# Kernel optimization log

Measured on AMD Instinct MI355X. Metric: run time of the kernel, lower is better.

Reference implementation:

```python
import jax, jax.numpy as jnp
import numpy as np

B, T, C = 1, 4096, 1024
NH, NKV, HD = 16, 4, 64
N_REP = NH // NKV
WIN = 1024
EPS = 1e-5
ROPE_THETA = 10000.0


def setup_inputs() -> dict:
    key = jax.random.key(0)
    ks = jax.random.split(key, 6)
    s = 1.0 / np.sqrt(C)
    x = jax.random.normal(ks[0], (B, T, C), jnp.float32)
    wq = jax.random.normal(ks[1], (NH * HD, C), jnp.float32) * s
    wk = jax.random.normal(ks[2], (NKV * HD, C), jnp.float32) * s
    wv = jax.random.normal(ks[3], (NKV * HD, C), jnp.float32) * s
    wo = jax.random.normal(ks[4], (C, NH * HD), jnp.float32) * (1.0 / np.sqrt(NH * HD))
    q_norm_w = jnp.ones((HD,), jnp.float32)
    k_norm_w = jnp.ones((HD,), jnp.float32)
    # RoPE tables: (T, HD//2)
    inv_freq = 1.0 / (ROPE_THETA ** (np.arange(0, HD, 2, dtype=np.float32) / HD))
    ang = np.outer(np.arange(T, dtype=np.float32), inv_freq)
    freqs_cos = jnp.asarray(np.cos(ang), jnp.float32)
    freqs_sin = jnp.asarray(np.sin(ang), jnp.float32)
    return {"x": x, "wq": wq, "wk": wk, "wv": wv, "wo": wo,
            "q_norm_w": q_norm_w, "k_norm_w": k_norm_w,
            "freqs_cos": freqs_cos, "freqs_sin": freqs_sin}


def _rmsnorm(v, w):
    # RMSNorm over last dim (per-head)
    return v * jax.lax.rsqrt(jnp.mean(v * v, axis=-1, keepdims=True) + EPS) * w


def _rope(v, cos, sin):
    # v: (B, T, H, HD); interleaved complex rotation, matching torch polar freqs_cis
    vr, vi = v[..., 0::2], v[..., 1::2]
    c = cos[None, :, None, :]
    s = sin[None, :, None, :]
    out_r = vr * c - vi * s
    out_i = vr * s + vi * c
    return jnp.stack([out_r, out_i], axis=-1).reshape(v.shape)


def reference(x, wq, wk, wv, wo, q_norm_w, k_norm_w, freqs_cos, freqs_sin):
    xq = jnp.einsum('btc,dc->btd', x, wq).reshape(B, T, NH, HD)
    xk = jnp.einsum('btc,dc->btd', x, wk).reshape(B, T, NKV, HD)
    xv = jnp.einsum('btc,dc->btd', x, wv).reshape(B, T, NKV, HD)
    # per-head QK RMSNorm
    xq = _rmsnorm(xq, q_norm_w)
    xk = _rmsnorm(xk, k_norm_w)
    # RoPE
    xq = _rope(xq, freqs_cos, freqs_sin)
    xk = _rope(xk, freqs_cos, freqs_sin)
    # GQA: expand kv heads
    xk = jnp.repeat(xk, N_REP, axis=2)  # (B, T, NH, HD)
    xv = jnp.repeat(xv, N_REP, axis=2)
    scale = 1.0 / np.sqrt(HD)
    scores = jnp.einsum('bthd,bshd->bhts', xq, xk) * scale
    i = jnp.arange(T)[:, None]
    j = jnp.arange(T)[None, :]
    mask = (i >= j) & (i - j < WIN)  # causal + sliding window
    scores = jnp.where(mask[None, None], scores, -jnp.inf)
    attn = jax.nn.softmax(scores, axis=-1)
    y = jnp.einsum('bhts,bshd->bthd', attn, xv).reshape(B, T, NH * HD)
    return jnp.einsum('btd,cd->btc', y, wo)
```

## Files before the change

kernel.cpp:

```cpp
#include <hip/hip_runtime.h>
#include <hip/hip_bf16.h>


#define WIN_SZ 1024

typedef __attribute__((ext_vector_type(8))) short short8;
typedef __attribute__((ext_vector_type(8))) unsigned short ushort8;
typedef __attribute__((ext_vector_type(4))) float f32x4;
typedef __attribute__((ext_vector_type(16))) float f32x16;

#define GLOAD_LDS16(g, s)                                              \
  __builtin_amdgcn_global_load_lds(                                    \
      (const __attribute__((address_space(1))) unsigned int*)(g),      \
      (__attribute__((address_space(3))) unsigned int*)(s), 16, 0, 0)

__device__ __forceinline__ unsigned short f2bf(float f) {
  union { float f; unsigned u; } v; v.f = f;
  unsigned r = v.u + 0x7fffu + ((v.u >> 16) & 1u);
  return (unsigned short)(r >> 16);
}

__device__ __forceinline__ float bf2f(unsigned short b) {
  union { unsigned u; float f; } v; v.u = ((unsigned)b) << 16; return v.f;
}

__device__ __forceinline__ unsigned pk2bf(float lo, float hi) {
  __hip_bfloat162 h = __float22bfloat162_rn(make_float2(lo, hi));
  union { __hip_bfloat162 h; unsigned u; } c; c.h = h; return c.u;
}

__device__ __forceinline__ short8 frag4(unsigned w0, unsigned w1, unsigned w2, unsigned w3) {
  union { unsigned u[4]; short8 s; } x;
  x.u[0] = w0; x.u[1] = w1; x.u[2] = w2; x.u[3] = w3; return x.s;
}

__global__ __launch_bounds__(256) void k_f2b_all(const float* __restrict__ x,
                                                 const float* __restrict__ wq,
                                                 const float* __restrict__ wk,
                                                 const float* __restrict__ wv,
                                                 const float* __restrict__ wo,
                                                 unsigned short* __restrict__ xb,
                                                 unsigned short* __restrict__ wqkvb,
                                                 unsigned short* __restrict__ wob) {
  int q = blockIdx.x * 256 + threadIdx.x;
  const float* src;
  unsigned short* dst;
  int off;
  if (q < 1048576) { src = x; dst = xb; off = q; }
  else if (q < 1310720) { src = wq; dst = wqkvb; off = q - 1048576; }
  else if (q < 1376256) { src = wk; dst = wqkvb + 1024 * 1024; off = q - 1310720; }
  else if (q < 1441792) { src = wv; dst = wqkvb + 1280 * 1024; off = q - 1376256; }
  else { src = wo; dst = wob; off = q - 1441792; }
  float4 v = ((const float4*)src)[off];
  ushort4 o;
  o.x = f2bf(v.x); o.y = f2bf(v.y); o.z = f2bf(v.z); o.w = f2bf(v.w);
  ((ushort4*)dst)[off] = o;
}

template <int BF16OUT>
__global__ __launch_bounds__(256) void k_gemmN64(const unsigned short* __restrict__ A,
                                                 const unsigned short* __restrict__ B,
                                                 void* __restrict__ Cv,
                                                 int M, int N, int K, int nblk) {
  __shared__ unsigned short As[2][128 * 64];
  __shared__ unsigned short Bs[2][64 * 64];
  const int id = blockIdx.x;
  const int chunk = gridDim.x >> 3;
  const int swz = (id & 7) * chunk + (id >> 3);
  const int n_idx = swz % nblk, m_idx = swz / nblk;
  const int m0 = m_idx * 128, n0 = n_idx * 64;

  const int tid = threadIdx.x;
  const int w = tid >> 6, l = tid & 63;
  const int wr = w >> 1, wc = w & 1;
  const int r = l & 15, g = l >> 4;
  const int lr = l >> 3, lc = l & 7;
  const int srowb = w * 32, browb = w * 16;

  f32x4 acc[4][2];
#pragma unroll
  for (int i = 0; i < 4; i++)
#pragma unroll
    for (int j = 0; j < 2; j++) acc[i][j] = {0.f, 0.f, 0.f, 0.f};

  const unsigned short* Ag = A + (size_t)(m0 + srowb + lr) * K + lc * 8;
  const unsigned short* Bg = B + (size_t)(n0 + browb + lr) * K + lc * 8;

  auto stage = [&](int buf, int k0) {
#pragma unroll
    for (int it = 0; it < 4; it++)
      GLOAD_LDS16(Ag + (size_t)(it * 8) * K + k0, &As[buf][(srowb + it * 8) * 64]);
#pragma unroll
    for (int it = 0; it < 2; it++)
      GLOAD_LDS16(Bg + (size_t)(it * 8) * K + k0, &Bs[buf][(browb + it * 8) * 64]);
  };

  stage(0, 0);
  __syncthreads();
  int cur = 0;
  const int NT = K >> 6;
  for (int t = 0; t < NT; ++t) {
    if (t + 1 < NT) stage(cur ^ 1, (t + 1) << 6);
    const char* Ab = (const char*)As[cur];
    const char* Bb = (const char*)Bs[cur];
#pragma unroll
    for (int kk = 0; kk < 2; kk++) {
      short8 af[4], bfr[2];
#pragma unroll
      for (int mi = 0; mi < 4; mi++)
        af[mi] = *(const short8*)(Ab + (wr * 64 + mi * 16 + r) * 128 + kk * 64 + g * 16);
#pragma unroll
      for (int nj = 0; nj < 2; nj++)
        bfr[nj] = *(const short8*)(Bb + (wc * 32 + nj * 16 + r) * 128 + kk * 64 + g * 16);
#pragma unroll
      for (int mi = 0; mi < 4; mi++)
#pragma unroll
        for (int nj = 0; nj < 2; nj++)
          acc[mi][nj] = __builtin_amdgcn_mfma_f32_16x16x32_bf16(af[mi], bfr[nj], acc[mi][nj], 0, 0, 0);
    }
    __syncthreads();
    cur ^= 1;
  }

#pragma unroll
  for (int mi = 0; mi < 4; mi++)
#pragma unroll
    for (int nj = 0; nj < 2; nj++) {
      int row = m0 + wr * 64 + mi * 16 + g * 4;
      int col = n0 + wc * 32 + nj * 16 + r;
      if (BF16OUT) {
        unsigned short* C = (unsigned short*)Cv;
#pragma unroll
        for (int e = 0; e < 4; e++)
          C[(size_t)(row + e) * N + col] = f2bf(acc[mi][nj][e]);
      } else {
        float* C = (float*)Cv;
#pragma unroll
        for (int e = 0; e < 4; e++)
          C[(size_t)(row + e) * N + col] = acc[mi][nj][e];
      }
    }
}

__global__ __launch_bounds__(256) void k_normrope(const unsigned short* __restrict__ QKV,
                                                  const float* __restrict__ qw,
                                                  const float* __restrict__ kw,
                                                  const float* __restrict__ fc,
                                                  const float* __restrict__ fs,
                                                  unsigned short* __restrict__ Qb,
                                                  unsigned short* __restrict__ Kb,
                                                  unsigned short* __restrict__ Vtg,
                                                  int* __restrict__ ctr) {
  if (blockIdx.x == 0 && threadIdx.x == 0) *ctr = 0;
  int gid = blockIdx.x * 4 + (threadIdx.x >> 6);
  int l = threadIdx.x & 63;
  int t = gid / 24;
  int u = gid - t * 24;
  if (u < 16) {
    float v = bf2f(QKV[(size_t)t * 1536 + u * 64 + l]);
    float ss = v * v;
#pragma unroll
    for (int off = 32; off; off >>= 1) ss += __shfl_xor(ss, off);
    float rms = rsqrtf(ss * (1.0f / 64.0f) + 1e-5f);
    float vn = v * rms * qw[l];
    float c = fc[t * 32 + (l >> 1)], s = fs[t * 32 + (l >> 1)];
    float p = __shfl_xor(vn, 1);
    float out = (l & 1) ? (p * s + vn * c) : (vn * c - p * s);
    Qb[(size_t)t * 1024 + u * 64 + l] = f2bf(out * 0.1803368801111204f);
  } else if (u < 20) {
    int hh = u - 16;
    float v = bf2f(QKV[(size_t)t * 1536 + 1024 + hh * 64 + l]);
    float ss = v * v;
#pragma unroll
    for (int off = 32; off; off >>= 1) ss += __shfl_xor(ss, off);
    float rms = rsqrtf(ss * (1.0f / 64.0f) + 1e-5f);
    float vn = v * rms * kw[l];
    float c = fc[t * 32 + (l >> 1)], s = fs[t * 32 + (l >> 1)];
    float p = __shfl_xor(vn, 1);
    float out = (l & 1) ? (p * s + vn * c) : (vn * c - p * s);
    Kb[(size_t)t * 256 + hh * 64 + l] = f2bf(out);
  } else {
    int hh = u - 20;
    Vtg[(size_t)(hh * 64 + l) * 4096 + t] = QKV[(size_t)t * 1536 + 1280 + hh * 64 + l];
  }
}

__global__ __launch_bounds__(512, 4) void k_attn5(const unsigned short* __restrict__ Qb,
                                                  const unsigned short* __restrict__ Kb,
                                                  const unsigned short* __restrict__ Vtg,
                                                  unsigned short* __restrict__ Yb,
                                                  int* __restrict__ ctr) {
  __shared__ char smem[4 * 8192 + 1024];
  __shared__ int s_unit;
  char* stage = smem;
  float* Obuf = (float*)smem;
  float* ml = (float*)(smem + 32768);

  const int tid = threadIdx.x, w = tid >> 6, l = tid & 63;
  const int hh = w & 3, half = w >> 2;
  const int l31 = l & 31, hi = l >> 5, l15 = l & 15;

  const int sb = tid >> 7;
  const int su = tid & 127;
  const int srow = su >> 1;
  const int sg = (su & 1) * 4;
  const int sbase = sb * 8192 + (srow & 31) * 256;
  const int srx = (srow & 15) << 4;
  const int srh = (srow >> 5) * 128;
  const bool isV = sb & 1;
  const int kbase = half * 16384;
  const int vbase = kbase + 8192;

  for (;;) {
    __syncthreads();
    if (tid == 0) s_unit = atomicAdd(ctr, 1);
    __syncthreads();
    const int u = s_unit;
    if (u >= 512) break;
    const int qi = 127 - (u >> 2);
    const int hk = u & 3;
    const int q0 = qi * 32;
    const int h = hk * 4 + hh;
    const int qrow = q0 + l31;

    int jlo = q0 - (WIN_SZ - 1);
    if (jlo < 0) jlo = 0;
    jlo &= ~63;
    const int jlast = ((q0 + 31) >> 6) << 6;
    const int nt = ((jlast - jlo) >> 6) + 1;
    const int nh0 = (nt + 1) >> 1;

    const unsigned short* gK = Kb + (size_t)srow * 256 + hk * 64 + sg * 8;
    const unsigned short* gV = Vtg + (size_t)(hk * 64 + srow) * 4096 + sg * 8;

    short8 qf[4];
#pragma unroll
    for (int ks = 0; ks < 4; ks++)
      qf[ks] = *(const short8*)(Qb + (size_t)qrow * 1024 + h * 64 + ks * 16 + hi * 8);

    f32x16 accO0, accO1;
#pragma unroll
    for (int i = 0; i < 16; i++) { accO0[i] = 0.f; accO1[i] = 0.f; }
    float m = -1e30f, lsum = 0.f;

    ushort8 pre[4];
    auto prefetch = [&](int s) {
      int jt0 = jlo + (s << 6);
      int t1 = nh0 + s;
      int jt1 = (t1 < nt) ? (jlo + (t1 << 6)) : jlo;
      int jt = (sb >= 2) ? jt1 : jt0;
      if (!isV) {
        const unsigned short* g = gK + (size_t)jt * 256;
#pragma unroll
        for (int e = 0; e < 4; e++) pre[e] = *(const ushort8*)(g + e * 8);
      } else {
        const unsigned short* g = gV + jt;
#pragma unroll
        for (int e = 0; e < 4; e++) pre[e] = *(const ushort8*)(g + e * 8);
      }
    };
    prefetch(0);

    for (int s = 0; s < nh0; ++s) {
      __syncthreads();
#pragma unroll
      for (int e = 0; e < 4; e++) {
        int dst = sbase + ((srh + (sg + e) * 16) ^ srx);
        *(ushort8*)(stage + dst) = pre[e];
      }
      __syncthreads();
      if (s + 1 < nh0) prefetch(s + 1);

      const int myt = half ? (nh0 + s) : s;
      if (myt < nt) {
        const int jt = jlo + (myt << 6);

        f32x16 st0, st1;
#pragma unroll
        for (int i = 0; i < 16; i++) { st0[i] = 0.f; st1[i] = 0.f; }
        __builtin_amdgcn_s_setprio(1);
#pragma unroll
        for (int ks = 0; ks < 4; ks++) {
          int colb = ks * 32 + hi * 16;
          short8 kf0 = *(const short8*)(stage + kbase + l31 * 256 + (colb ^ (l15 << 4)));
          st0 = __builtin_amdgcn_mfma_f32_32x32x16_bf16(kf0, qf[ks], st0, 0, 0, 0);
          short8 kf1 = *(const short8*)(stage + kbase + l31 * 256 + ((128 + colb) ^ (l15 << 4)));
          st1 = __builtin_amdgcn_mfma_f32_32x32x16_bf16(kf1, qf[ks], st1, 0, 0, 0);
        }
        __builtin_amdgcn_s_setprio(0);

        if (jt + 63 > q0 || (q0 + 31) - jt >= WIN_SZ) {
          const int jb = jt + hi * 4;
#pragma unroll
          for (int rg = 0; rg < 16; rg++) {
            int j0 = jb + (rg & 3) + 8 * (rg >> 2);
            if (!((j0 <= qrow) && (qrow - j0 < WIN_SZ))) st0[rg] = -3.0e38f;
            int j1 = j0 + 32;
            if (!((j1 <= qrow) && (qrow - j1 < WIN_SZ))) st1[rg] = -3.0e38f;
          }
        }

        float mx = st0[0];
#pragma unroll
        for (int rg = 1; rg < 16; rg++) mx = fmaxf(mx, st0[rg]);
#pragma unroll
        for (int rg = 0; rg < 16; rg++) mx = fmaxf(mx, st1[rg]);
        mx = fmaxf(mx, __shfl_xor(mx, 32));
        if (!__all(mx <= m + 8.0f)) {
          float mnew = fmaxf(m, mx);
          float alpha = exp2f(m - mnew);
#pragma unroll
          for (int rg = 0; rg < 16; rg++) { accO0[rg] *= alpha; accO1[rg] *= alpha; }
          lsum *= alpha;
          m = mnew;
        }
        float ps = 0.f;
#pragma unroll
        for (int rg = 0; rg < 16; rg++) { st0[rg] = exp2f(st0[rg] - m); ps += st0[rg]; }
#pragma unroll
        for (int rg = 0; rg < 16; rg++) { st1[rg] = exp2f(st1[rg] - m); ps += st1[rg]; }
        lsum += ps;

        unsigned pd0[2][4], pd1[2][4];
#pragma unroll
        for (int b = 0; b < 4; b++) {
          pd0[0][b] = pk2bf(st0[4 * b], st0[4 * b + 1]);
          pd1[0][b] = pk2bf(st0[4 * b + 2], st0[4 * b + 3]);
          pd0[1][b] = pk2bf(st1[4 * b], st1[4 * b + 1]);
          pd1[1][b] = pk2bf(st1[4 * b + 2], st1[4 * b + 3]);
        }

        __builtin_amdgcn_s_setprio(1);
#pragma unroll
        for (int jj = 0; jj < 2; jj++) {
#pragma unroll
          for (int ks2 = 0; ks2 < 2; ks2++) {
            unsigned a0 = pd0[jj][2 * ks2], a1 = pd0[jj][2 * ks2 + 1];
            unsigned b0 = pd1[jj][2 * ks2], b1 = pd1[jj][2 * ks2 + 1];
            unsigned a0x = __shfl_xor(a0, 32), a1x = __shfl_xor(a1, 32);
            unsigned b0x = __shfl_xor(b0, 32), b1x = __shfl_xor(b1, 32);
            unsigned w0 = hi ? a1x : a0;
            unsigned w1 = hi ? b1x : b0;
            unsigned w2 = hi ? a1 : a0x;
            unsigned w3 = hi ? b1 : b0x;
            short8 pf = frag4(w0, w1, w2, w3);
            int colb2 = jj * 64 + ks2 * 32 + hi * 16;
            short8 vf0 = *(const short8*)(stage + vbase + l31 * 256 + (colb2 ^ (l15 << 4)));
            accO0 = __builtin_amdgcn_mfma_f32_32x32x16_bf16(vf0, pf, accO0, 0, 0, 0);
            short8 vf1 = *(const short8*)(stage + vbase + l31 * 256 + ((128 + colb2) ^ (l15 << 4)));
            accO1 = __builtin_amdgcn_mfma_f32_32x32x16_bf16(vf1, pf, accO1, 0, 0, 0);
          }
        }
        __builtin_amdgcn_s_setprio(0);
      }
    }

    lsum += __shfl_xor(lsum, 32);
    __syncthreads();
    if (half == 1) {
#pragma unroll
      for (int dd = 0; dd < 2; dd++) {
        const f32x16& a = dd ? accO1 : accO0;
#pragma unroll
        for (int rg = 0; rg < 16; rg++) {
          int d = dd * 32 + 8 * (rg >> 2) + 4 * hi + (rg & 3);
          Obuf[(hh * 64 + d) * 32 + l31] = a[rg];
        }
      }
      if (!hi) { ml[(hh * 2 + 0) * 32 + l31] = m; ml[(hh * 2 + 1) * 32 + l31] = lsum; }
    }
    __syncthreads();
    if (half == 0) {
      float m1 = ml[(hh * 2 + 0) * 32 + l31];
      float l1 = ml[(hh * 2 + 1) * 32 + l31];
      float ms = fmaxf(m, m1);
      float a0 = exp2f(m - ms), a1 = exp2f(m1 - ms);
      float inv = 1.0f / (lsum * a0 + l1 * a1);
      a0 *= inv; a1 *= inv;
#pragma unroll
      for (int dd = 0; dd < 2; dd++) {
        const f32x16& a = dd ? accO1 : accO0;
#pragma unroll
        for (int b = 0; b < 4; b++) {
          float o[4];
#pragma unroll
          for (int e = 0; e < 4; e++) {
            int d = dd * 32 + 8 * b + 4 * hi + e;
            o[e] = a[4 * b + e] * a0 + Obuf[(hh * 64 + d) * 32 + l31] * a1;
          }
          union { unsigned uu[2]; ushort4 v; } ov;
          ov.uu[0] = pk2bf(o[0], o[1]);
          ov.uu[1] = pk2bf(o[2], o[3]);
          *(ushort4*)(Yb + (size_t)qrow * 1024 + h * 64 + dd * 32 + b * 8 + hi * 4) = ov.v;
        }
      }
    }
  }
}

extern "C" void kernel_launch(void* const* d_in, const int* in_sizes, int n_in,
                              void* d_out, int out_size, void* d_ws, size_t ws_size,
                              hipStream_t stream) {
  const float* x = (const float*)d_in[0];
  const float* wq = (const float*)d_in[1];
  const float* wk = (const float*)d_in[2];
  const float* wv = (const float*)d_in[3];
  const float* wo = (const float*)d_in[4];
  const float* qw = (const float*)d_in[5];
  const float* kw = (const float*)d_in[6];
  const float* fc = (const float*)d_in[7];
  const float* fs = (const float*)d_in[8];
  float* out = (float*)d_out;

  char* p = (char*)d_ws;
  auto alloc = [&](size_t b) {
    char* q = p;
    p += (b + 255) & ~(size_t)255;
    return q;
  };
  unsigned short* xb = (unsigned short*)alloc((size_t)4096 * 1024 * 2);
  unsigned short* wqkvb = (unsigned short*)alloc((size_t)1536 * 1024 * 2);
  unsigned short* wob = (unsigned short*)alloc((size_t)1024 * 1024 * 2);
  unsigned short* QKVb = (unsigned short*)alloc((size_t)4096 * 1536 * 2);
  unsigned short* Qb = (unsigned short*)alloc((size_t)4096 * 1024 * 2);
  unsigned short* Kb = (unsigned short*)alloc((size_t)4096 * 256 * 2);
  unsigned short* Vtg = (unsigned short*)alloc((size_t)256 * 4096 * 2);
  unsigned short* Yb = (unsigned short*)alloc((size_t)4096 * 1024 * 2);
  int* ctr = (int*)alloc(256);

  k_f2b_all<<<6656, 256, 0, stream>>>(x, wq, wk, wv, wo, xb, wqkvb, wob);
  k_gemmN64<1><<<768, 256, 0, stream>>>(xb, wqkvb, QKVb, 4096, 1536, 1024, 24);
  k_normrope<<<24576, 256, 0, stream>>>(QKVb, qw, kw, fc, fs, Qb, Kb, Vtg, ctr);
  k_attn5<<<384, 512, 0, stream>>>(Qb, Kb, Vtg, Yb, ctr);
  k_gemmN64<0><<<512, 256, 0, stream>>>(Yb, wob, out, 4096, 1024, 1024, 16);
}
```

Measured before the change: 135.0 us.

## Replace persistent atomic scheduler with static pairing and double-buffered LDS staging

The attention kernel drops its persistent atomic work queue and launches one block per (query tile, kv head) unit. Each block id maps to a unit so that long and short causal tiles are paired. K/V staging now uses two LDS buffers of 32KB each, so the next tile is stored while the current one is computed, which removes one barrier per iteration. The cost is twice the LDS footprint per block, which may limit how many blocks fit on a CU, and the static mapping may balance work less evenly than the dynamic queue.

```diff
diff --git a/kernel.cpp b/kernel.cpp
--- a/kernel.cpp
+++ b/kernel.cpp
@@ -149,9 +149,7 @@
                                                   const float* __restrict__ fs,
                                                   unsigned short* __restrict__ Qb,
                                                   unsigned short* __restrict__ Kb,
-                                                  unsigned short* __restrict__ Vtg,
-                                                  int* __restrict__ ctr) {
-  if (blockIdx.x == 0 && threadIdx.x == 0) *ctr = 0;
+                                                  unsigned short* __restrict__ Vtg) {
   int gid = blockIdx.x * 4 + (threadIdx.x >> 6);
   int l = threadIdx.x & 63;
   int t = gid / 24;
@@ -185,20 +183,34 @@
   }
 }
 
-__global__ __launch_bounds__(512, 4) void k_attn5(const unsigned short* __restrict__ Qb,
+__global__ __launch_bounds__(512, 4) void k_attn6(const unsigned short* __restrict__ Qb,
                                                   const unsigned short* __restrict__ Kb,
                                                   const unsigned short* __restrict__ Vtg,
-                                                  unsigned short* __restrict__ Yb,
-                                                  int* __restrict__ ctr) {
-  __shared__ char smem[4 * 8192 + 1024];
-  __shared__ int s_unit;
+                                                  unsigned short* __restrict__ Yb) {
+  __shared__ char smem[65536 + 1024];
   char* stage = smem;
   float* Obuf = (float*)smem;
-  float* ml = (float*)(smem + 32768);
+  float* ml = (float*)(smem + 65536);
+
+  const int id = blockIdx.x;
+  const int cupair = id & 255, sel = id >> 8;
+  int qi = cupair >> 1;
+  if (sel) qi = 127 - qi;
+  const int hk = (cupair & 1) * 2 + sel;
+  const int q0 = qi * 32;
 
   const int tid = threadIdx.x, w = tid >> 6, l = tid & 63;
   const int hh = w & 3, half = w >> 2;
+  const int h = hk * 4 + hh;
   const int l31 = l & 31, hi = l >> 5, l15 = l & 15;
+  const int qrow = q0 + l31;
+
+  int jlo = q0 - (WIN_SZ - 1);
+  if (jlo < 0) jlo = 0;
+  jlo &= ~63;
+  const int jlast = ((q0 + 31) >> 6) << 6;
+  const int nt = ((jlast - jlo) >> 6) + 1;
+  const int nh0 = (nt + 1) >> 1;
 
   const int sb = tid >> 7;
   const int su = tid & 127;
@@ -208,191 +220,177 @@
   const int srx = (srow & 15) << 4;
   const int srh = (srow >> 5) * 128;
   const bool isV = sb & 1;
-  const int kbase = half * 16384;
-  const int vbase = kbase + 8192;
-
-  for (;;) {
+  const unsigned short* gK = Kb + (size_t)srow * 256 + hk * 64 + sg * 8;
+  const unsigned short* gV = Vtg + (size_t)(hk * 64 + srow) * 4096 + sg * 8;
+
+  short8 qf[4];
+#pragma unroll
+  for (int ks = 0; ks < 4; ks++)
+    qf[ks] = *(const short8*)(Qb + (size_t)qrow * 1024 + h * 64 + ks * 16 + hi * 8);
+
+  f32x16 accO0, accO1;
+#pragma unroll
+  for (int i = 0; i < 16; i++) { accO0[i] = 0.f; accO1[i] = 0.f; }
+  float m = -1e30f, lsum = 0.f;
+
+  ushort8 pre[4];
+  auto prefetch = [&](int s) {
+    int jt0 = jlo + (s << 6);
+    int t1 = nh0 + s;
+    int jt1 = (t1 < nt) ? (jlo + (t1 << 6)) : jlo;
+    int jt = (sb >= 2) ? jt1 : jt0;
+    if (!isV) {
+      const unsigned short* g = gK + (size_t)jt * 256;
+#pragma unroll
+      for (int e = 0; e < 4; e++) pre[e] = *(const ushort8*)(g + e * 8);
+    } else {
+      const unsigned short* g = gV + jt;
+#pragma unroll
+      for (int e = 0; e < 4; e++) pre[e] = *(const ushort8*)(g + e * 8);
+    }
+  };
+  auto store_set = [&](int set) {
+    char* dstb = stage + set * 32768 + sbase;
+#pragma unroll
+    for (int e = 0; e < 4; e++)
+      *(ushort8*)(dstb + ((srh + (sg + e) * 16) ^ srx)) = pre[e];
+  };
+
+  prefetch(0);
+  store_set(0);
+  if (nh0 > 1) prefetch(1);
+  __syncthreads();
+
+  for (int s = 0; s < nh0; ++s) {
+    if (s + 1 < nh0) {
+      store_set((s + 1) & 1);
+      if (s + 2 < nh0) prefetch(s + 2);
+    }
+    const int setoff = (s & 1) * 32768;
+    const int kbase = setoff + half * 16384;
+    const int vbase = kbase + 8192;
+
+    const int myt = half ? (nh0 + s) : s;
+    if (myt < nt) {
+      const int jt = jlo + (myt << 6);
+
+      f32x16 st0, st1;
+#pragma unroll
+      for (int i = 0; i < 16; i++) { st0[i] = 0.f; st1[i] = 0.f; }
+      __builtin_amdgcn_s_setprio(1);
+#pragma unroll
+      for (int ks = 0; ks < 4; ks++) {
+        int colb = ks * 32 + hi * 16;
+        short8 kf0 = *(const short8*)(stage + kbase + l31 * 256 + (colb ^ (l15 << 4)));
+        st0 = __builtin_amdgcn_mfma_f32_32x32x16_bf16(kf0, qf[ks], st0, 0, 0, 0);
+        short8 kf1 = *(const short8*)(stage + kbase + l31 * 256 + ((128 + colb) ^ (l15 << 4)));
+        st1 = __builtin_amdgcn_mfma_f32_32x32x16_bf16(kf1, qf[ks], st1, 0, 0, 0);
+      }
+      __builtin_amdgcn_s_setprio(0);
+
+      if (jt + 63 > q0 || (q0 + 31) - jt >= WIN_SZ) {
+        const int jb = jt + hi * 4;
+#pragma unroll
+        for (int rg = 0; rg < 16; rg++) {
+          int j0 = jb + (rg & 3) + 8 * (rg >> 2);
+          if (!((j0 <= qrow) && (qrow - j0 < WIN_SZ))) st0[rg] = -3.0e38f;
+          int j1 = j0 + 32;
+          if (!((j1 <= qrow) && (qrow - j1 < WIN_SZ))) st1[rg] = -3.0e38f;
+        }
+      }
+
+      float mx = st0[0];
+#pragma unroll
+      for (int rg = 1; rg < 16; rg++) mx = fmaxf(mx, st0[rg]);
+#pragma unroll
+      for (int rg = 0; rg < 16; rg++) mx = fmaxf(mx, st1[rg]);
+      mx = fmaxf(mx, __shfl_xor(mx, 32));
+      if (!__all(mx <= m + 8.0f)) {
+        float mnew = fmaxf(m, mx);
+        float alpha = exp2f(m - mnew);
+#pragma unroll
+        for (int rg = 0; rg < 16; rg++) { accO0[rg] *= alpha; accO1[rg] *= alpha; }
+        lsum *= alpha;
+        m = mnew;
+      }
+      float ps = 0.f;
+#pragma unroll
+      for (int rg = 0; rg < 16; rg++) { st0[rg] = exp2f(st0[rg] - m); ps += st0[rg]; }
+#pragma unroll
+      for (int rg = 0; rg < 16; rg++) { st1[rg] = exp2f(st1[rg] - m); ps += st1[rg]; }
+      lsum += ps;
+
+      unsigned pd0[2][4], pd1[2][4];
+#pragma unroll
+      for (int b = 0; b < 4; b++) {
+        pd0[0][b] = pk2bf(st0[4 * b], st0[4 * b + 1]);
+        pd1[0][b] = pk2bf(st0[4 * b + 2], st0[4 * b + 3]);
+        pd0[1][b] = pk2bf(st1[4 * b], st1[4 * b + 1]);
+        pd1[1][b] = pk2bf(st1[4 * b + 2], st1[4 * b + 3]);
+      }
+
+      __builtin_amdgcn_s_setprio(1);
+#pragma unroll
+      for (int jj = 0; jj < 2; jj++) {
+#pragma unroll
+        for (int ks2 = 0; ks2 < 2; ks2++) {
+          unsigned a0 = pd0[jj][2 * ks2], a1 = pd0[jj][2 * ks2 + 1];
+          unsigned b0 = pd1[jj][2 * ks2], b1 = pd1[jj][2 * ks2 + 1];
+          unsigned a0x = __shfl_xor(a0, 32), a1x = __shfl_xor(a1, 32);
+          unsigned b0x = __shfl_xor(b0, 32), b1x = __shfl_xor(b1, 32);
+          unsigned w0 = hi ? a1x : a0;
+          unsigned w1 = hi ? b1x : b0;
+          unsigned w2 = hi ? a1 : a0x;
+          unsigned w3 = hi ? b1 : b0x;
+          short8 pf = frag4(w0, w1, w2, w3);
+          int colb2 = jj * 64 + ks2 * 32 + hi * 16;
+          short8 vf0 = *(const short8*)(stage + vbase + l31 * 256 + (colb2 ^ (l15 << 4)));
+          accO0 = __builtin_amdgcn_mfma_f32_32x32x16_bf16(vf0, pf, accO0, 0, 0, 0);
+          short8 vf1 = *(const short8*)(stage + vbase + l31 * 256 + ((128 + colb2) ^ (l15 << 4)));
+          accO1 = __builtin_amdgcn_mfma_f32_32x32x16_bf16(vf1, pf, accO1, 0, 0, 0);
+        }
+      }
+      __builtin_amdgcn_s_setprio(0);
+    }
     __syncthreads();
-    if (tid == 0) s_unit = atomicAdd(ctr, 1);
-    __syncthreads();
-    const int u = s_unit;
-    if (u >= 512) break;
-    const int qi = 127 - (u >> 2);
-    const int hk = u & 3;
-    const int q0 = qi * 32;
-    const int h = hk * 4 + hh;
-    const int qrow = q0 + l31;
-
-    int jlo = q0 - (WIN_SZ - 1);
-    if (jlo < 0) jlo = 0;
-    jlo &= ~63;
-    const int jlast = ((q0 + 31) >> 6) << 6;
-    const int nt = ((jlast - jlo) >> 6) + 1;
-    const int nh0 = (nt + 1) >> 1;
-
-    const unsigned short* gK = Kb + (size_t)srow * 256 + hk * 64 + sg * 8;
-    const unsigned short* gV = Vtg + (size_t)(hk * 64 + srow) * 4096 + sg * 8;
-
-    short8 qf[4];
-#pragma unroll
-    for (int ks = 0; ks < 4; ks++)
-      qf[ks] = *(const short8*)(Qb + (size_t)qrow * 1024 + h * 64 + ks * 16 + hi * 8);
-
-    f32x16 accO0, accO1;
-#pragma unroll
-    for (int i = 0; i < 16; i++) { accO0[i] = 0.f; accO1[i] = 0.f; }
-    float m = -1e30f, lsum = 0.f;
-
-    ushort8 pre[4];
-    auto prefetch = [&](int s) {
-      int jt0 = jlo + (s << 6);
-      int t1 = nh0 + s;
-      int jt1 = (t1 < nt) ? (jlo + (t1 << 6)) : jlo;
-      int jt = (sb >= 2) ? jt1 : jt0;
-      if (!isV) {
-        const unsigned short* g = gK + (size_t)jt * 256;
-#pragma unroll
-        for (int e = 0; e < 4; e++) pre[e] = *(const ushort8*)(g + e * 8);
-      } else {
-        const unsigned short* g = gV + jt;
-#pragma unroll
-        for (int e = 0; e < 4; e++) pre[e] = *(const ushort8*)(g + e * 8);
-      }
-    };
-    prefetch(0);
-
-    for (int s = 0; s < nh0; ++s) {
-      __syncthreads();
-#pragma unroll
-      for (int e = 0; e < 4; e++) {
-        int dst = sbase + ((srh + (sg + e) * 16) ^ srx);
-        *(ushort8*)(stage + dst) = pre[e];
-      }
-      __syncthreads();
-      if (s + 1 < nh0) prefetch(s + 1);
-
-      const int myt = half ? (nh0 + s) : s;
-      if (myt < nt) {
-        const int jt = jlo + (myt << 6);
-
-        f32x16 st0, st1;
-#pragma unroll
-        for (int i = 0; i < 16; i++) { st0[i] = 0.f; st1[i] = 0.f; }
-        __builtin_amdgcn_s_setprio(1);
-#pragma unroll
-        for (int ks = 0; ks < 4; ks++) {
-          int colb = ks * 32 + hi * 16;
-          short8 kf0 = *(const short8*)(stage + kbase + l31 * 256 + (colb ^ (l15 << 4)));
-          st0 = __builtin_amdgcn_mfma_f32_32x32x16_bf16(kf0, qf[ks], st0, 0, 0, 0);
-          short8 kf1 = *(const short8*)(stage + kbase + l31 * 256 + ((128 + colb) ^ (l15 << 4)));
-          st1 = __builtin_amdgcn_mfma_f32_32x32x16_bf16(kf1, qf[ks], st1, 0, 0, 0);
+  }
+
+  lsum += __shfl_xor(lsum, 32);
+  if (half == 1) {
+#pragma unroll
+    for (int dd = 0; dd < 2; dd++) {
+      const f32x16& a = dd ? accO1 : accO0;
+#pragma unroll
+      for (int rg = 0; rg < 16; rg++) {
+        int d = dd * 32 + 8 * (rg >> 2) + 4 * hi + (rg & 3);
+        Obuf[(hh * 64 + d) * 32 + l31] = a[rg];
+      }
+    }
+    if (!hi) { ml[(hh * 2 + 0) * 32 + l31] = m; ml[(hh * 2 + 1) * 32 + l31] = lsum; }
+  }
+  __syncthreads();
+  if (half == 0) {
+    float m1 = ml[(hh * 2 + 0) * 32 + l31];
+    float l1 = ml[(hh * 2 + 1) * 32 + l31];
+    float ms = fmaxf(m, m1);
+    float a0 = exp2f(m - ms), a1 = exp2f(m1 - ms);
+    float inv = 1.0f / (lsum * a0 + l1 * a1);
+    a0 *= inv; a1 *= inv;
+#pragma unroll
+    for (int dd = 0; dd < 2; dd++) {
+      const f32x16& a = dd ? accO1 : accO0;
+#pragma unroll
+      for (int b = 0; b < 4; b++) {
+        float o[4];
+#pragma unroll
+        for (int e = 0; e < 4; e++) {
+          int d = dd * 32 + 8 * b + 4 * hi + e;
+          o[e] = a[4 * b + e] * a0 + Obuf[(hh * 64 + d) * 32 + l31] * a1;
         }
-        __builtin_amdgcn_s_setprio(0);
-
-        if (jt + 63 > q0 || (q0 + 31) - jt >= WIN_SZ) {
-          const int jb = jt + hi * 4;
-#pragma unroll
-          for (int rg = 0; rg < 16; rg++) {
-            int j0 = jb + (rg & 3) + 8 * (rg >> 2);
-            if (!((j0 <= qrow) && (qrow - j0 < WIN_SZ))) st0[rg] = -3.0e38f;
-            int j1 = j0 + 32;
-            if (!((j1 <= qrow) && (qrow - j1 < WIN_SZ))) st1[rg] = -3.0e38f;
-          }
-        }
-
-        float mx = st0[0];
-#pragma unroll
-        for (int rg = 1; rg < 16; rg++) mx = fmaxf(mx, st0[rg]);
-#pragma unroll
-        for (int rg = 0; rg < 16; rg++) mx = fmaxf(mx, st1[rg]);
-        mx = fmaxf(mx, __shfl_xor(mx, 32));
-        if (!__all(mx <= m + 8.0f)) {
-          float mnew = fmaxf(m, mx);
-          float alpha = exp2f(m - mnew);
-#pragma unroll
-          for (int rg = 0; rg < 16; rg++) { accO0[rg] *= alpha; accO1[rg] *= alpha; }
-          lsum *= alpha;
-          m = mnew;
-        }
-        float ps = 0.f;
-#pragma unroll
-        for (int rg = 0; rg < 16; rg++) { st0[rg] = exp2f(st0[rg] - m); ps += st0[rg]; }
-#pragma unroll
-        for (int rg = 0; rg < 16; rg++) { st1[rg] = exp2f(st1[rg] - m); ps += st1[rg]; }
-        lsum += ps;
-
-        unsigned pd0[2][4], pd1[2][4];
-#pragma unroll
-        for (int b = 0; b < 4; b++) {
-          pd0[0][b] = pk2bf(st0[4 * b], st0[4 * b + 1]);
-          pd1[0][b] = pk2bf(st0[4 * b + 2], st0[4 * b + 3]);
-          pd0[1][b] = pk2bf(st1[4 * b], st1[4 * b + 1]);
-          pd1[1][b] = pk2bf(st1[4 * b + 2], st1[4 * b + 3]);
-        }
-
-        __builtin_amdgcn_s_setprio(1);
-#pragma unroll
-        for (int jj = 0; jj < 2; jj++) {
-#pragma unroll
-          for (int ks2 = 0; ks2 < 2; ks2++) {
-            unsigned a0 = pd0[jj][2 * ks2], a1 = pd0[jj][2 * ks2 + 1];
-            unsigned b0 = pd1[jj][2 * ks2], b1 = pd1[jj][2 * ks2 + 1];
-            unsigned a0x = __shfl_xor(a0, 32), a1x = __shfl_xor(a1, 32);
-            unsigned b0x = __shfl_xor(b0, 32), b1x = __shfl_xor(b1, 32);
-            unsigned w0 = hi ? a1x : a0;
-            unsigned w1 = hi ? b1x : b0;
-            unsigned w2 = hi ? a1 : a0x;
-            unsigned w3 = hi ? b1 : b0x;
-            short8 pf = frag4(w0, w1, w2, w3);
-            int colb2 = jj * 64 + ks2 * 32 + hi * 16;
-            short8 vf0 = *(const short8*)(stage + vbase + l31 * 256 + (colb2 ^ (l15 << 4)));
-            accO0 = __builtin_amdgcn_mfma_f32_32x32x16_bf16(vf0, pf, accO0, 0, 0, 0);
-            short8 vf1 = *(const short8*)(stage + vbase + l31 * 256 + ((128 + colb2) ^ (l15 << 4)));
-            accO1 = __builtin_amdgcn_mfma_f32_32x32x16_bf16(vf1, pf, accO1, 0, 0, 0);
-          }
-        }
-        __builtin_amdgcn_s_setprio(0);
-      }
-    }
-
-    lsum += __shfl_xor(lsum, 32);
-    __syncthreads();
-    if (half == 1) {
-#pragma unroll
-      for (int dd = 0; dd < 2; dd++) {
-        const f32x16& a = dd ? accO1 : accO0;
-#pragma unroll
-        for (int rg = 0; rg < 16; rg++) {
-          int d = dd * 32 + 8 * (rg >> 2) + 4 * hi + (rg & 3);
-          Obuf[(hh * 64 + d) * 32 + l31] = a[rg];
-        }
-      }
-      if (!hi) { ml[(hh * 2 + 0) * 32 + l31] = m; ml[(hh * 2 + 1) * 32 + l31] = lsum; }
-    }
-    __syncthreads();
-    if (half == 0) {
-      float m1 = ml[(hh * 2 + 0) * 32 + l31];
-      float l1 = ml[(hh * 2 + 1) * 32 + l31];
-      float ms = fmaxf(m, m1);
-      float a0 = exp2f(m - ms), a1 = exp2f(m1 - ms);
-      float inv = 1.0f / (lsum * a0 + l1 * a1);
-      a0 *= inv; a1 *= inv;
-#pragma unroll
-      for (int dd = 0; dd < 2; dd++) {
-        const f32x16& a = dd ? accO1 : accO0;
-#pragma unroll
-        for (int b = 0; b < 4; b++) {
-          float o[4];
-#pragma unroll
-          for (int e = 0; e < 4; e++) {
-            int d = dd * 32 + 8 * b + 4 * hi + e;
-            o[e] = a[4 * b + e] * a0 + Obuf[(hh * 64 + d) * 32 + l31] * a1;
-          }
-          union { unsigned uu[2]; ushort4 v; } ov;
-          ov.uu[0] = pk2bf(o[0], o[1]);
-          ov.uu[1] = pk2bf(o[2], o[3]);
-          *(ushort4*)(Yb + (size_t)qrow * 1024 + h * 64 + dd * 32 + b * 8 + hi * 4) = ov.v;
-        }
+        union { unsigned uu[2]; ushort4 v; } ov;
+        ov.uu[0] = pk2bf(o[0], o[1]);
+        ov.uu[1] = pk2bf(o[2], o[3]);
+        *(ushort4*)(Yb + (size_t)qrow * 1024 + h * 64 + dd * 32 + b * 8 + hi * 4) = ov.v;
       }
     }
   }
@@ -426,11 +424,10 @@
   unsigned short* Kb = (unsigned short*)alloc((size_t)4096 * 256 * 2);
   unsigned short* Vtg = (unsigned short*)alloc((size_t)256 * 4096 * 2);
   unsigned short* Yb = (unsigned short*)alloc((size_t)4096 * 1024 * 2);
-  int* ctr = (int*)alloc(256);
 
   k_f2b_all<<<6656, 256, 0, stream>>>(x, wq, wk, wv, wo, xb, wqkvb, wob);
   k_gemmN64<1><<<768, 256, 0, stream>>>(xb, wqkvb, QKVb, 4096, 1536, 1024, 24);
-  k_normrope<<<24576, 256, 0, stream>>>(QKVb, qw, kw, fc, fs, Qb, Kb, Vtg, ctr);
-  k_attn5<<<384, 512, 0, stream>>>(Qb, Kb, Vtg, Yb, ctr);
+  k_normrope<<<24576, 256, 0, stream>>>(QKVb, qw, kw, fc, fs, Qb, Kb, Vtg);
+  k_attn6<<<512, 512, 0, stream>>>(Qb, Kb, Vtg, Yb);
   k_gemmN64<0><<<512, 256, 0, stream>>>(Yb, wob, out, 4096, 1024, 1024, 16);
 }
```

Result: faster. 121.0 us (-10.4%).
